# Performance work log

Hardware: AMD Instinct MI355X
Metric: run time of the kernel (lower is better)

The kernel has to match this reference:

```python
import jax, jax.numpy as jnp
import numpy as np

N_NODES = 100000
N_EDGES = 2000000
D_IN = 4
HID = 64


def setup_inputs() -> dict:
    key = jax.random.key(0)
    ks = jax.random.split(key, 8)
    node_feats = jax.random.normal(ks[0], (N_NODES, D_IN), dtype=jnp.float32)
    pairs = jax.random.randint(ks[1], (N_EDGES, 2), 0, N_NODES, dtype=jnp.int64)
    # Kaiming-ish init scaling
    W1 = jax.random.normal(ks[2], (D_IN, HID), dtype=jnp.float32) / np.sqrt(D_IN)
    b1 = jnp.zeros((HID,), dtype=jnp.float32)
    W2 = jax.random.normal(ks[3], (HID, HID), dtype=jnp.float32) / np.sqrt(HID)
    b2 = jnp.zeros((HID,), dtype=jnp.float32)
    We1 = jax.random.normal(ks[4], (3 * HID, HID), dtype=jnp.float32) / np.sqrt(3 * HID)
    be1 = jnp.zeros((HID,), dtype=jnp.float32)
    We2 = jax.random.normal(ks[5], (HID, 1), dtype=jnp.float32) / np.sqrt(HID)
    be2 = jnp.zeros((1,), dtype=jnp.float32)
    return {"node_feats": node_feats, "pairs": pairs, "W1": W1, "b1": b1,
            "W2": W2, "b2": b2, "We1": We1, "be1": be1, "We2": We2, "be2": be2}


def reference(node_feats, pairs, W1, b1, W2, b2, We1, be1, We2, be2):
    # node MLP: Linear -> ReLU -> Linear -> ReLU
    H = jax.nn.relu(node_feats @ W1 + b1)      # [N, HID]
    H = jax.nn.relu(H @ W2 + b2)               # [N, HID]
    # vectorized gather over all edge pairs (replaces Python loop)
    hu = H[pairs[:, 0]]                        # [E, HID]
    hv = H[pairs[:, 1]]                        # [E, HID]
    E = jnp.concatenate([hu, hv, jnp.abs(hu - hv)], axis=-1)  # [E, 3*HID]
    # edge MLP: Linear -> ReLU -> Linear, squeeze last dim
    scores = (jax.nn.relu(E @ We1 + be1) @ We2 + be2)[:, 0]   # [E]
    return scores
```

## Files before the change

kernel.cpp:

```cpp
#include <hip/hip_runtime.h>

#define N_NODES 100000
#define N_EDGES 2000000

typedef __bf16 bf16x8 __attribute__((ext_vector_type(8)));
typedef float f32x4 __attribute__((ext_vector_type(4)));
typedef float f32x16 __attribute__((ext_vector_type(16)));

#define AS1 __attribute__((address_space(1)))
#define AS3 __attribute__((address_space(3)))

struct TrueTag { static constexpr bool value = true; };
struct FalseTag { static constexpr bool value = false; };

__device__ __forceinline__ unsigned f2bf_rne(float f) {
  unsigned u = __builtin_bit_cast(unsigned, f);
  u += 0x7FFFu + ((u >> 16) & 1u);
  return u >> 16;
}

__device__ __forceinline__ unsigned pack_rhu(float lo, float hi) {
  unsigned ulo = __builtin_bit_cast(unsigned, lo) + 0x8000u;
  unsigned uhi = __builtin_bit_cast(unsigned, hi) + 0x8000u;
  return __builtin_amdgcn_perm(uhi, ulo, 0x07060302u);
}

__device__ __forceinline__ unsigned absdiff_pack(unsigned a, unsigned b) {
  float alo = __builtin_bit_cast(float, a << 16);
  float ahi = __builtin_bit_cast(float, a & 0xFFFF0000u);
  float blo = __builtin_bit_cast(float, b << 16);
  float bhi = __builtin_bit_cast(float, b & 0xFFFF0000u);
  return pack_rhu(fabsf(alo - blo), fabsf(ahi - bhi));
}

__global__ __launch_bounds__(64, 1) void node_mfma_kernel(
    const float* __restrict__ X, const float* __restrict__ W1,
    const float* __restrict__ b1, const float* __restrict__ W2,
    const float* __restrict__ b2, unsigned short* __restrict__ H) {
  const int lane = threadIdx.x;
  const int l15 = lane & 15;
  const int quad = lane >> 4;

  float w1v[2][4][8], b1v[2][8];
#pragma unroll
  for (int c = 0; c < 2; ++c)
#pragma unroll
    for (int j = 0; j < 8; ++j) {
      int col = c * 32 + quad * 8 + j;
      b1v[c][j] = b1[col];
#pragma unroll
      for (int d = 0; d < 4; ++d) w1v[c][d][j] = W1[d * 64 + col];
    }

  uint4 afr[2][4];
#pragma unroll
  for (int c = 0; c < 2; ++c)
#pragma unroll
    for (int mt = 0; mt < 4; ++mt) {
      unsigned w[4];
#pragma unroll
      for (int p = 0; p < 4; ++p) {
        int k = c * 32 + quad * 8 + 2 * p;
        unsigned lo = f2bf_rne(W2[k * 64 + mt * 16 + l15]);
        unsigned hi = f2bf_rne(W2[(k + 1) * 64 + mt * 16 + l15]);
        w[p] = lo | (hi << 16);
      }
      afr[c][mt] = make_uint4(w[0], w[1], w[2], w[3]);
    }
  float b2v[16];
#pragma unroll
  for (int mt = 0; mt < 4; ++mt)
#pragma unroll
    for (int r = 0; r < 4; ++r) b2v[mt * 4 + r] = b2[mt * 16 + quad * 4 + r];

  const int ntiles = N_NODES / 16;
  for (int tile = blockIdx.x; tile < ntiles; tile += gridDim.x) {
    float4 xv = ((const float4*)X)[tile * 16 + l15];

    uint4 bfr[2];
#pragma unroll
    for (int c = 0; c < 2; ++c) {
      unsigned w[4];
#pragma unroll
      for (int p = 0; p < 4; ++p) {
        float h0 = fmaxf(b1v[c][2 * p] + xv.x * w1v[c][0][2 * p] +
                             xv.y * w1v[c][1][2 * p] + xv.z * w1v[c][2][2 * p] +
                             xv.w * w1v[c][3][2 * p],
                         0.f);
        float h1 = fmaxf(b1v[c][2 * p + 1] + xv.x * w1v[c][0][2 * p + 1] +
                             xv.y * w1v[c][1][2 * p + 1] +
                             xv.z * w1v[c][2][2 * p + 1] +
                             xv.w * w1v[c][3][2 * p + 1],
                         0.f);
        w[p] = pack_rhu(h0, h1);
      }
      bfr[c] = make_uint4(w[0], w[1], w[2], w[3]);
    }

    f32x4 acc[4];
#pragma unroll
    for (int mt = 0; mt < 4; ++mt) acc[mt] = (f32x4){0.f, 0.f, 0.f, 0.f};
#pragma unroll
    for (int c = 0; c < 2; ++c)
#pragma unroll
      for (int mt = 0; mt < 4; ++mt)
        acc[mt] = __builtin_amdgcn_mfma_f32_16x16x32_bf16(
            __builtin_bit_cast(bf16x8, afr[c][mt]),
            __builtin_bit_cast(bf16x8, bfr[c]), acc[mt], 0, 0, 0);

    unsigned short* hrow = H + (tile * 16 + l15) * 64;
#pragma unroll
    for (int mt = 0; mt < 4; ++mt) {
      unsigned lo = pack_rhu(fmaxf(acc[mt][0] + b2v[mt * 4 + 0], 0.f),
                             fmaxf(acc[mt][1] + b2v[mt * 4 + 1], 0.f));
      unsigned hi = pack_rhu(fmaxf(acc[mt][2] + b2v[mt * 4 + 2], 0.f),
                             fmaxf(acc[mt][3] + b2v[mt * 4 + 3], 0.f));
      *(uint2*)(hrow + mt * 16 + quad * 4) = make_uint2(lo, hi);
    }
  }
}

__global__ __launch_bounds__(256, 3) void edge_mlp_kernel(
    const unsigned short* __restrict__ H, const int* __restrict__ pairs,
    const float* __restrict__ We1, const float* __restrict__ be1,
    const float* __restrict__ We2, const float* __restrict__ be2,
    float* __restrict__ out) {
  __shared__ uint4 gbuf[4][512];
  __shared__ uint4 lds_w6[6][2][64];
  __shared__ float lds_c[64];

  const int tid = threadIdx.x;
  const int lane = tid & 63;
  const int n = lane & 31;
  const int half = lane >> 5;
  const int wave = tid >> 6;
  const int rowsel = lane >> 3;
  const int swzc = (lane & 7) ^ rowsel;

  if (tid < 64) lds_c[tid] = We2[tid];

#pragma unroll
  for (int i = 0; i < 3; ++i) {
    const int idx = wave * 3 + i;
    const int c = 6 + (idx >> 1);
    const int mt = idx & 1;
    const int col = mt * 32 + n;
    const int kb = c * 16 + half * 8;
    unsigned w[4];
#pragma unroll
    for (int p = 0; p < 4; ++p)
      w[p] = f2bf_rne(We1[(kb + 2 * p) * 64 + col]) |
             (f2bf_rne(We1[(kb + 2 * p + 1) * 64 + col]) << 16);
    lds_w6[c - 6][mt][lane] = make_uint4(w[0], w[1], w[2], w[3]);
  }

  uint4 afr[6][2];
#pragma unroll
  for (int c = 0; c < 6; ++c)
#pragma unroll
    for (int mt = 0; mt < 2; ++mt) {
      const int col = mt * 32 + n;
      const int kb = c * 16 + half * 8;
      unsigned w[4];
#pragma unroll
      for (int p = 0; p < 4; ++p)
        w[p] = f2bf_rne(We1[(kb + 2 * p) * 64 + col]) |
               (f2bf_rne(We1[(kb + 2 * p + 1) * 64 + col]) << 16);
      afr[c][mt] = make_uint4(w[0], w[1], w[2], w[3]);
    }
  unsigned a12[2];
#pragma unroll
  for (int mt = 0; mt < 2; ++mt)
    a12[mt] = (half == 0) ? f2bf_rne(be1[mt * 32 + n]) : 0u;
  const uint4 b13u = make_uint4((half == 0) ? 0x00003F80u : 0u, 0u, 0u, 0u);
  const float be2v = be2[0];

  uint4* const buf = &gbuf[wave][0];
  int rbo[4];
#pragma unroll
  for (int c = 0; c < 4; ++c) rbo[c] = n * 8 + ((2 * c + half) ^ (n & 7));

  const int wid = blockIdx.x * 4 + wave;
  const int nw = gridDim.x * 4;
  const int ntiles = N_EDGES / 32;
  const int last = ntiles - 1;
  const int2* pairs2 = (const int2*)pairs;

  __syncthreads();

  auto issue_gathers = [&](uint4* dst, const int2* prs) {
#pragma unroll
    for (int k = 0; k < 4; ++k) {
      const AS1 unsigned* gu =
          (const AS1 unsigned*)(H + (size_t)prs[k].x * 64) + swzc * 4;
      const AS1 unsigned* gv =
          (const AS1 unsigned*)(H + (size_t)prs[k].y * 64) + swzc * 4;
      __builtin_amdgcn_global_load_lds(gu, (AS3 unsigned*)(dst + k * 64), 16,
                                       0, 0);
      __builtin_amdgcn_global_load_lds(
          gv, (AS3 unsigned*)(dst + 256 + k * 64), 16, 0, 0);
    }
  };

  int2 pr[4];
  {
#pragma unroll
    for (int k = 0; k < 4; ++k) pr[k] = pairs2[wid * 32 + k * 8 + rowsel];
    issue_gathers(buf, pr);
    __builtin_amdgcn_sched_barrier(0);
    int t1 = wid + nw <= last ? wid + nw : last;
#pragma unroll
    for (int k = 0; k < 4; ++k) pr[k] = pairs2[t1 * 32 + k * 8 + rowsel];
  }

  auto body = [&](int tc, auto FIRST) {
    __builtin_amdgcn_sched_barrier(0);
    if constexpr (decltype(FIRST)::value)
      __builtin_amdgcn_s_waitcnt(0x0F74);
    else
      __builtin_amdgcn_s_waitcnt(0x0F75);
    __builtin_amdgcn_sched_barrier(0);

    const int t = tc <= last ? tc : last;
    uint4 hu[4], hv[4];
#pragma unroll
    for (int c = 0; c < 4; ++c) {
      hu[c] = buf[rbo[c]];
      hv[c] = buf[256 + rbo[c]];
    }
    asm volatile("s_waitcnt lgkmcnt(0)" ::: "memory");
    __builtin_amdgcn_sched_barrier(0);
    issue_gathers(buf, pr);
    __builtin_amdgcn_sched_barrier(0);
    {
      int tn = tc + 2 * nw <= last ? tc + 2 * nw : last;
#pragma unroll
      for (int k = 0; k < 4; ++k) pr[k] = pairs2[tn * 32 + k * 8 + rowsel];
    }

    uint4 ab[4];
#pragma unroll
    for (int c = 0; c < 4; ++c) {
      ab[c].x = absdiff_pack(hu[c].x, hv[c].x);
      ab[c].y = absdiff_pack(hu[c].y, hv[c].y);
      ab[c].z = absdiff_pack(hu[c].z, hv[c].z);
      ab[c].w = absdiff_pack(hu[c].w, hv[c].w);
    }

    f32x16 acc[2];
    acc[0] = (f32x16)(0.f);
    acc[1] = (f32x16)(0.f);
#pragma unroll
    for (int c = 0; c < 4; ++c) {
      const bf16x8 b = __builtin_bit_cast(bf16x8, hu[c]);
#pragma unroll
      for (int mt = 0; mt < 2; ++mt)
        acc[mt] = __builtin_amdgcn_mfma_f32_32x32x16_bf16(
            __builtin_bit_cast(bf16x8, afr[c][mt]), b, acc[mt], 0, 0, 0);
    }
#pragma unroll
    for (int c = 0; c < 2; ++c) {
      const bf16x8 b = __builtin_bit_cast(bf16x8, hv[c]);
#pragma unroll
      for (int mt = 0; mt < 2; ++mt)
        acc[mt] = __builtin_amdgcn_mfma_f32_32x32x16_bf16(
            __builtin_bit_cast(bf16x8, afr[4 + c][mt]), b, acc[mt], 0, 0, 0);
    }
#pragma unroll
    for (int c = 0; c < 2; ++c) {
      const bf16x8 b = __builtin_bit_cast(bf16x8, hv[2 + c]);
#pragma unroll
      for (int mt = 0; mt < 2; ++mt) {
        const uint4 a = lds_w6[c][mt][lane];
        acc[mt] = __builtin_amdgcn_mfma_f32_32x32x16_bf16(
            __builtin_bit_cast(bf16x8, a), b, acc[mt], 0, 0, 0);
      }
    }
#pragma unroll
    for (int c = 0; c < 4; ++c) {
      const bf16x8 b = __builtin_bit_cast(bf16x8, ab[c]);
#pragma unroll
      for (int mt = 0; mt < 2; ++mt) {
        const uint4 a = lds_w6[2 + c][mt][lane];
        acc[mt] = __builtin_amdgcn_mfma_f32_32x32x16_bf16(
            __builtin_bit_cast(bf16x8, a), b, acc[mt], 0, 0, 0);
      }
    }
#pragma unroll
    for (int mt = 0; mt < 2; ++mt)
      acc[mt] = __builtin_amdgcn_mfma_f32_32x32x16_bf16(
          __builtin_bit_cast(bf16x8, make_uint4(a12[mt], 0u, 0u, 0u)),
          __builtin_bit_cast(bf16x8, b13u), acc[mt], 0, 0, 0);

    float s = 0.f;
#pragma unroll
    for (int mt = 0; mt < 2; ++mt)
#pragma unroll
      for (int g = 0; g < 4; ++g) {
        const float4 ew = *(const float4*)&lds_c[mt * 32 + g * 8 + 4 * half];
        s += fmaxf(acc[mt][4 * g + 0], 0.f) * ew.x;
        s += fmaxf(acc[mt][4 * g + 1], 0.f) * ew.y;
        s += fmaxf(acc[mt][4 * g + 2], 0.f) * ew.z;
        s += fmaxf(acc[mt][4 * g + 3], 0.f) * ew.w;
      }
    s += __shfl_xor(s, 32);
    if (half == 0) out[t * 32 + n] = s + be2v;
  };

  int t = wid;
  body(t, TrueTag{});
  for (t += nw; t < ntiles; t += nw) body(t, FalseTag{});
}

extern "C" void kernel_launch(void* const* d_in, const int* in_sizes, int n_in,
                              void* d_out, int out_size, void* d_ws,
                              size_t ws_size, hipStream_t stream) {
  const float* X = (const float*)d_in[0];
  const int* pairs = (const int*)d_in[1];
  const float* W1 = (const float*)d_in[2];
  const float* b1 = (const float*)d_in[3];
  const float* W2 = (const float*)d_in[4];
  const float* b2 = (const float*)d_in[5];
  const float* We1 = (const float*)d_in[6];
  const float* be1 = (const float*)d_in[7];
  const float* We2 = (const float*)d_in[8];
  const float* be2 = (const float*)d_in[9];
  float* out = (float*)d_out;
  unsigned short* H = (unsigned short*)d_ws;

  node_mfma_kernel<<<1024, 64, 0, stream>>>(X, W1, b1, W2, b2, H);
  edge_mlp_kernel<<<768, 256, 0, stream>>>(H, pairs, We1, be1, We2, be2, out);
}
```

Baseline: 156.6 us.

## Replace abs-diff with packed min via |a-b| = a+b-2min(a,b) identity

Because H is post-ReLU and non-negative, |hu-hv| equals hu+hv-2*min(hu,hv), and min of non-negative bf16 values can be taken as an unsigned 16-bit integer min. The first-layer edge weights are folded so the hu and hv blocks absorb the abs-diff weights and the third block carries -2x. This replaces per-element float unpack, subtract, abs and repack with a single packed integer min, reducing VALU work in the edge loop. Folding the weights before bf16 rounding changes numerics slightly. The node kernel grid is also raised from 1024 to 3125 blocks.

```diff
diff --git a/kernel.cpp b/kernel.cpp
--- a/kernel.cpp
+++ b/kernel.cpp
@@ -6,6 +6,7 @@
 typedef __bf16 bf16x8 __attribute__((ext_vector_type(8)));
 typedef float f32x4 __attribute__((ext_vector_type(4)));
 typedef float f32x16 __attribute__((ext_vector_type(16)));
+typedef unsigned short u16x2 __attribute__((ext_vector_type(2)));
 
 #define AS1 __attribute__((address_space(1)))
 #define AS3 __attribute__((address_space(3)))
@@ -25,12 +26,10 @@
   return __builtin_amdgcn_perm(uhi, ulo, 0x07060302u);
 }
 
-__device__ __forceinline__ unsigned absdiff_pack(unsigned a, unsigned b) {
-  float alo = __builtin_bit_cast(float, a << 16);
-  float ahi = __builtin_bit_cast(float, a & 0xFFFF0000u);
-  float blo = __builtin_bit_cast(float, b << 16);
-  float bhi = __builtin_bit_cast(float, b & 0xFFFF0000u);
-  return pack_rhu(fabsf(alo - blo), fabsf(ahi - bhi));
+__device__ __forceinline__ unsigned pk_min_u16(unsigned a, unsigned b) {
+  u16x2 r = __builtin_elementwise_min(__builtin_bit_cast(u16x2, a),
+                                      __builtin_bit_cast(u16x2, b));
+  return __builtin_bit_cast(unsigned, r);
 }
 
 __global__ __launch_bounds__(64, 1) void node_mfma_kernel(
@@ -139,6 +138,13 @@
 
   if (tid < 64) lds_c[tid] = We2[tid];
 
+  auto wcomb = [&](int c, int kk, int col) -> float {
+    const float w = We1[kk * 64 + col];
+    if (c < 4) return w + We1[(kk + 128) * 64 + col];
+    if (c < 8) return w + We1[(kk + 64) * 64 + col];
+    return -2.f * w;
+  };
+
 #pragma unroll
   for (int i = 0; i < 3; ++i) {
     const int idx = wave * 3 + i;
@@ -149,8 +155,8 @@
     unsigned w[4];
 #pragma unroll
     for (int p = 0; p < 4; ++p)
-      w[p] = f2bf_rne(We1[(kb + 2 * p) * 64 + col]) |
-             (f2bf_rne(We1[(kb + 2 * p + 1) * 64 + col]) << 16);
+      w[p] = f2bf_rne(wcomb(c, kb + 2 * p, col)) |
+             (f2bf_rne(wcomb(c, kb + 2 * p + 1, col)) << 16);
     lds_w6[c - 6][mt][lane] = make_uint4(w[0], w[1], w[2], w[3]);
   }
 
@@ -164,8 +170,8 @@
       unsigned w[4];
 #pragma unroll
       for (int p = 0; p < 4; ++p)
-        w[p] = f2bf_rne(We1[(kb + 2 * p) * 64 + col]) |
-               (f2bf_rne(We1[(kb + 2 * p + 1) * 64 + col]) << 16);
+        w[p] = f2bf_rne(wcomb(c, kb + 2 * p, col)) |
+               (f2bf_rne(wcomb(c, kb + 2 * p + 1, col)) << 16);
       afr[c][mt] = make_uint4(w[0], w[1], w[2], w[3]);
     }
   unsigned a12[2];
@@ -238,13 +244,13 @@
       for (int k = 0; k < 4; ++k) pr[k] = pairs2[tn * 32 + k * 8 + rowsel];
     }
 
-    uint4 ab[4];
+    uint4 pmn[4];
 #pragma unroll
     for (int c = 0; c < 4; ++c) {
-      ab[c].x = absdiff_pack(hu[c].x, hv[c].x);
-      ab[c].y = absdiff_pack(hu[c].y, hv[c].y);
-      ab[c].z = absdiff_pack(hu[c].z, hv[c].z);
-      ab[c].w = absdiff_pack(hu[c].w, hv[c].w);
+      pmn[c].x = pk_min_u16(hu[c].x, hv[c].x);
+      pmn[c].y = pk_min_u16(hu[c].y, hv[c].y);
+      pmn[c].z = pk_min_u16(hu[c].z, hv[c].z);
+      pmn[c].w = pk_min_u16(hu[c].w, hv[c].w);
     }
 
     f32x16 acc[2];
@@ -278,7 +284,7 @@
     }
 #pragma unroll
     for (int c = 0; c < 4; ++c) {
-      const bf16x8 b = __builtin_bit_cast(bf16x8, ab[c]);
+      const bf16x8 b = __builtin_bit_cast(bf16x8, pmn[c]);
 #pragma unroll
       for (int mt = 0; mt < 2; ++mt) {
         const uint4 a = lds_w6[2 + c][mt][lane];
@@ -328,6 +334,6 @@
   float* out = (float*)d_out;
   unsigned short* H = (unsigned short*)d_ws;
 
-  node_mfma_kernel<<<1024, 64, 0, stream>>>(X, W1, b1, W2, b2, H);
+  node_mfma_kernel<<<3125, 64, 0, stream>>>(X, W1, b1, W2, b2, H);
   edge_mlp_kernel<<<768, 256, 0, stream>>>(H, pairs, We1, be1, We2, be2, out);
 }
```

Measured after the change: 171.3 us. 9.4% more time.
